# Performance work log

Hardware: AMD Instinct MI355X
Metric: run time of the kernel (lower is better)

Reference implementation:

```python
import jax, jax.numpy as jnp
import numpy as np
from functools import partial

N_NODES = 50000
N_EDGES = 800000
IN_F, HID_F, OUT_F = 128, 128, 64


def _linear_params(key, in_f, out_f):
    k1, k2 = jax.random.split(key)
    bound = 1.0 / np.sqrt(in_f)
    W = jax.random.uniform(k1, (out_f, in_f), jnp.float32, -bound, bound)
    b = jax.random.uniform(k2, (out_f,), jnp.float32, -bound, bound)
    return W, b


def setup_inputs() -> dict:
    key = jax.random.key(0)
    ks = jax.random.split(key, 10)
    features = jax.random.normal(ks[0], (N_NODES, IN_F), jnp.float32)
    src = jax.random.randint(ks[1], (N_EDGES,), 0, N_NODES, jnp.int32)
    dst = jax.random.randint(ks[2], (N_EDGES,), 0, N_NODES, jnp.int32)
    W1a, b1a = _linear_params(ks[3], IN_F, HID_F)
    W1b, b1b = _linear_params(ks[4], HID_F, HID_F)
    W2a, b2a = _linear_params(ks[5], HID_F, HID_F)
    W2b, b2b = _linear_params(ks[6], HID_F, HID_F)
    W3a, b3a = _linear_params(ks[7], HID_F, HID_F)
    W3b, b3b = _linear_params(ks[8], HID_F, OUT_F)
    return dict(features=features, src=src, dst=dst,
                W1a=W1a, b1a=b1a, W1b=W1b, b1b=b1b,
                W2a=W2a, b2a=b2a, W2b=W2b, b2b=b2b,
                W3a=W3a, b3a=b3a, W3b=W3b, b3b=b3b)


def _mean_agg(x, src, dst, n_nodes):
    # gather src features, segment-sum into dst, divide by in-degree (0-deg -> 0)
    summed = jax.ops.segment_sum(x[src], dst, num_segments=n_nodes)
    deg = jax.ops.segment_sum(jnp.ones((src.shape[0],), x.dtype), dst,
                              num_segments=n_nodes)
    return summed / jnp.maximum(deg, 1.0)[:, None]


def _gin_conv(x, src, dst, Wa, ba, Wb, bb):
    # DGL GINConv, aggregator 'mean', eps=0: h = MLP((1+eps)*x + mean_agg)
    h = x + _mean_agg(x, src, dst, x.shape[0])
    h = jax.nn.relu(h @ Wa.T + ba)
    return h @ Wb.T + bb


def reference(features, src, dst,
              W1a, b1a, W1b, b1b,
              W2a, b2a, W2b, b2b,
              W3a, b3a, W3b, b3b):
    x = jax.nn.relu(_gin_conv(features, src, dst, W1a, b1a, W1b, b1b))
    x = jax.nn.relu(_gin_conv(x, src, dst, W2a, b2a, W2b, b2b))
    x = jax.nn.relu(x @ W3a.T + b3a)
    return x @ W3b.T + b3b
```

## Files before the change

### kernel.cpp

```cpp
#include <hip/hip_runtime.h>
#include <hip/hip_fp16.h>

#define N_NODES 50000
#define N_EDGES 800000

typedef __attribute__((ext_vector_type(8))) short bf16x8;
typedef __attribute__((ext_vector_type(4))) float f32x4;

#define OFF_BUFA   0UL
#define OFF_T16    25600000UL
#define OFF_CNT    38400000UL
#define OFF_W      38600064UL
#define OFF_CSR    38960512UL

#define NB_EDGE 3125
#define NB_W    352
#define NB_FEAT 6250

__device__ __forceinline__ unsigned short bf16_rne(float f) {
  unsigned u = __float_as_uint(f);
  unsigned r = (u + 0x7FFFu + ((u >> 16) & 1u)) >> 16;
  return (unsigned short)r;
}

__device__ __forceinline__ int swz(int row, int b) {
  return (row * 256 + b) ^ ((row & 7) << 4);
}

__global__ __launch_bounds__(256)
void scatter16(const int* __restrict__ src, const int* __restrict__ dst,
               int* __restrict__ cnt, unsigned short* __restrict__ csr) {
  int i = blockIdx.x * 256 + threadIdx.x;
  int d = dst[i];
  int pos = atomicAdd(&cnt[d], 1);
  if (pos < 64) csr[(d << 6) + pos] = (unsigned short)src[i];
}

__global__ __launch_bounds__(256)
void conv_kernel(const float* __restrict__ W1a, const float* __restrict__ W1b,
                 const float* __restrict__ W2a, const float* __restrict__ W2b,
                 const float* __restrict__ W3a, const float* __restrict__ W3b,
                 unsigned short* __restrict__ pool,
                 const float* __restrict__ feat, __half* __restrict__ t16) {
  const int b = blockIdx.x;
  const int tid = threadIdx.x;
  if (b < NB_W) {
    int i = b * 256 + tid;
    const float* s;
    int base, local, msize;
    if (i < 16384)      { s = W1a; base = 0;      local = i;          msize = 16384; }
    else if (i < 32768) { s = W1b; base = 32768;  local = i - 16384;  msize = 16384; }
    else if (i < 49152) { s = W2a; base = 65536;  local = i - 32768;  msize = 16384; }
    else if (i < 65536) { s = W2b; base = 98304;  local = i - 49152;  msize = 16384; }
    else if (i < 81920) { s = W3a; base = 131072; local = i - 65536;  msize = 16384; }
    else                { s = W3b; base = 163840; local = i - 81920;  msize = 8192;  }
    float f = s[local];
    unsigned short hi = bf16_rne(f);
    float fh = __uint_as_float((unsigned)hi << 16);
    pool[base + local] = hi;
    pool[base + msize + local] = bf16_rne(f - fh);
  } else {
    int i = (b - NB_W) * 1024 + tid * 4;
    float4 v = *reinterpret_cast<const float4*>(feat + i);
    ushort4 h;
    h.x = __half_as_ushort(__float2half_rn(v.x));
    h.y = __half_as_ushort(__float2half_rn(v.y));
    h.z = __half_as_ushort(__float2half_rn(v.z));
    h.w = __half_as_ushort(__float2half_rn(v.w));
    *reinterpret_cast<ushort4*>((unsigned short*)t16 + i) = h;
  }
}

template <bool SELF32>
__global__ __launch_bounds__(256)
void agg_kernel(const __half* __restrict__ t16, const float* __restrict__ xself,
                const unsigned short* __restrict__ csr, const int* __restrict__ cnt,
                float* __restrict__ out) {
  int node = blockIdx.x * 4 + (threadIdx.x >> 6);
  if (node >= N_NODES) return;
  const int lane = threadIdx.x & 63;
  int deg = cnt[node];
  int dloop = min(deg, 64);
  int beg = node << 6;
  float inv = 1.0f / fmaxf((float)deg, 1.0f);

  float s0 = 0.f, s1 = 0.f, t0 = 0.f, t1 = 0.f;
  float u0 = 0.f, u1 = 0.f, v0 = 0.f, v1 = 0.f;
  int e = 0;
  for (; e + 3 < dloop; e += 4) {
    ushort4 q = *reinterpret_cast<const ushort4*>(csr + beg + e);
    float2 a = __half22float2(*reinterpret_cast<const __half2*>(t16 + (size_t)q.x * 128 + lane * 2));
    float2 b = __half22float2(*reinterpret_cast<const __half2*>(t16 + (size_t)q.y * 128 + lane * 2));
    float2 c = __half22float2(*reinterpret_cast<const __half2*>(t16 + (size_t)q.z * 128 + lane * 2));
    float2 d = __half22float2(*reinterpret_cast<const __half2*>(t16 + (size_t)q.w * 128 + lane * 2));
    s0 += a.x; s1 += a.y; t0 += b.x; t1 += b.y;
    u0 += c.x; u1 += c.y; v0 += d.x; v1 += d.y;
  }
  for (; e < dloop; ++e) {
    int i0 = csr[beg + e];
    float2 a = __half22float2(*reinterpret_cast<const __half2*>(t16 + (size_t)i0 * 128 + lane * 2));
    s0 += a.x; s1 += a.y;
  }
  float2 sm = make_float2(s0 + t0 + u0 + v0, s1 + t1 + u1 + v1);
  float2 xv;
  if (SELF32) {
    xv = *reinterpret_cast<const float2*>(xself + (size_t)node * 128 + lane * 2);
  } else {
    xv = __half22float2(*reinterpret_cast<const __half2*>(t16 + (size_t)node * 128 + lane * 2));
  }
  float2 o = make_float2(fmaf(sm.x, inv, xv.x), fmaf(sm.y, inv, xv.y));
  *reinterpret_cast<float2*>(out + (size_t)node * 128 + lane * 2) = o;
}

__device__ __forceinline__ void stage_x32(const float* __restrict__ X, int m0, int tid,
                                          char* ahi, char* alo, int M) {
  #pragma unroll
  for (int it = 0; it < 4; ++it) {
    int f = tid + it * 256;
    int row = f >> 5, c = f & 31;
    float4 v = make_float4(0.f, 0.f, 0.f, 0.f);
    if (m0 + row < M)
      v = *reinterpret_cast<const float4*>(X + (size_t)(m0 + row) * 128 + c * 4);
    ushort4 hi, lo;
    float fh;
    hi.x = bf16_rne(v.x); fh = __uint_as_float((unsigned)hi.x << 16); lo.x = bf16_rne(v.x - fh);
    hi.y = bf16_rne(v.y); fh = __uint_as_float((unsigned)hi.y << 16); lo.y = bf16_rne(v.y - fh);
    hi.z = bf16_rne(v.z); fh = __uint_as_float((unsigned)hi.z << 16); lo.z = bf16_rne(v.z - fh);
    hi.w = bf16_rne(v.w); fh = __uint_as_float((unsigned)hi.w << 16); lo.w = bf16_rne(v.w - fh);
    int bo = swz(row, c * 8);
    *reinterpret_cast<ushort4*>(ahi + bo) = hi;
    *reinterpret_cast<ushort4*>(alo + bo) = lo;
  }
}

template <int NB>
__device__ __forceinline__ void load_bfrag(const unsigned short* __restrict__ Wh,
                                           const unsigned short* __restrict__ Wl,
                                           int w, int lrow, int lg,
                                           bf16x8 (&bh)[NB][4], bf16x8 (&bl)[NB][4]) {
  #pragma unroll
  for (int nb = 0; nb < NB; ++nb) {
    int col = w * (16 * NB) + nb * 16 + lrow;
    #pragma unroll
    for (int kk = 0; kk < 4; ++kk) {
      int idx = col * 128 + kk * 32 + lg * 8;
      bh[nb][kk] = *reinterpret_cast<const bf16x8*>(Wh + idx);
      bl[nb][kk] = *reinterpret_cast<const bf16x8*>(Wl + idx);
    }
  }
}

template <int NB>
__device__ __forceinline__ void gemm_lds32(const char* ahi, const char* alo, int lrow, int lg,
                                           const bf16x8 (&bh)[NB][4], const bf16x8 (&bl)[NB][4],
                                           f32x4 (&acc)[2][NB]) {
  #pragma unroll
  for (int i = 0; i < 2; ++i)
    #pragma unroll
    for (int nb = 0; nb < NB; ++nb) acc[i][nb] = (f32x4){0.f, 0.f, 0.f, 0.f};
  #pragma unroll
  for (int i = 0; i < 2; ++i) {
    #pragma unroll
    for (int kk = 0; kk < 4; ++kk) {
      int bo = swz(i * 16 + lrow, kk * 64 + lg * 16);
      bf16x8 ah = *reinterpret_cast<const bf16x8*>(ahi + bo);
      bf16x8 al = *reinterpret_cast<const bf16x8*>(alo + bo);
      #pragma unroll
      for (int nb = 0; nb < NB; ++nb) {
        acc[i][nb] = __builtin_amdgcn_mfma_f32_16x16x32_bf16(ah, bh[nb][kk], acc[i][nb], 0, 0, 0);
        acc[i][nb] = __builtin_amdgcn_mfma_f32_16x16x32_bf16(al, bh[nb][kk], acc[i][nb], 0, 0, 0);
        acc[i][nb] = __builtin_amdgcn_mfma_f32_16x16x32_bf16(ah, bl[nb][kk], acc[i][nb], 0, 0, 0);
      }
    }
  }
}

__device__ __forceinline__ void store_h32(char* ahi, char* alo, const float* __restrict__ bias,
                                          int w, int lrow, int lg, f32x4 (&acc)[2][2]) {
  #pragma unroll
  for (int i = 0; i < 2; ++i) {
    #pragma unroll
    for (int nb = 0; nb < 2; ++nb) {
      int col = w * 32 + nb * 16 + lrow;
      float b = bias[col];
      #pragma unroll
      for (int r = 0; r < 4; ++r) {
        float v = fmaxf(acc[i][nb][r] + b, 0.f);
        int row = i * 16 + lg * 4 + r;
        unsigned short h = bf16_rne(v);
        float fh = __uint_as_float((unsigned)h << 16);
        unsigned short l2 = bf16_rne(v - fh);
        int bo = swz(row, col * 2);
        *reinterpret_cast<unsigned short*>(ahi + bo) = h;
        *reinterpret_cast<unsigned short*>(alo + bo) = l2;
      }
    }
  }
}

__global__ __launch_bounds__(256)
void mlp1_kernel(const float* __restrict__ X, const unsigned short* __restrict__ p,
                 const float* __restrict__ b1a, const float* __restrict__ b1b,
                 __half* __restrict__ Y, int M) {
  __shared__ unsigned short Ahi[32 * 128];
  __shared__ unsigned short Alo[32 * 128];
  char* ahi = (char*)Ahi;
  char* alo = (char*)Alo;
  const int tid = threadIdx.x;
  const int w = tid >> 6, l = tid & 63;
  const int lrow = l & 15, lg = l >> 4;
  const int m0 = blockIdx.x * 32;

  stage_x32(X, m0, tid, ahi, alo, M);
  __syncthreads();

  f32x4 acc[2][2];
  {
    bf16x8 bh[2][4], bl[2][4];
    load_bfrag<2>(p + 0, p + 16384, w, lrow, lg, bh, bl);
    gemm_lds32<2>(ahi, alo, lrow, lg, bh, bl, acc);
  }
  __syncthreads();
  {
    bf16x8 bh[2][4], bl[2][4];
    load_bfrag<2>(p + 32768, p + 49152, w, lrow, lg, bh, bl);
    store_h32(ahi, alo, b1a, w, lrow, lg, acc);
    __syncthreads();
    gemm_lds32<2>(ahi, alo, lrow, lg, bh, bl, acc);
  }
  #pragma unroll
  for (int i = 0; i < 2; ++i) {
    #pragma unroll
    for (int nb = 0; nb < 2; ++nb) {
      int col = w * 32 + nb * 16 + lrow;
      float b = b1b[col];
      #pragma unroll
      for (int r = 0; r < 4; ++r) {
        float v = fmaxf(acc[i][nb][r] + b, 0.f);
        int row = m0 + i * 16 + lg * 4 + r;
        if (row < M) Y[(size_t)row * 128 + col] = __float2half_rn(v);
      }
    }
  }
}

__global__ __launch_bounds__(256)
void mlp2head_kernel(const float* __restrict__ X, const unsigned short* __restrict__ p,
                     const float* __restrict__ b2a, const float* __restrict__ b2b,
                     const float* __restrict__ b3a, const float* __restrict__ b3b,
                     float* __restrict__ Y, int M) {
  __shared__ unsigned short Ahi[32 * 128];
  __shared__ unsigned short Alo[32 * 128];
  char* ahi = (char*)Ahi;
  char* alo = (char*)Alo;
  const int tid = threadIdx.x;
  const int w = tid >> 6, l = tid & 63;
  const int lrow = l & 15, lg = l >> 4;
  const int m0 = blockIdx.x * 32;

  stage_x32(X, m0, tid, ahi, alo, M);
  __syncthreads();

  f32x4 acc[2][2];
  {
    bf16x8 bh[2][4], bl[2][4];
    load_bfrag<2>(p + 65536, p + 81920, w, lrow, lg, bh, bl);
    gemm_lds32<2>(ahi, alo, lrow, lg, bh, bl, acc);
  }
  __syncthreads();
  {
    bf16x8 bh[2][4], bl[2][4];
    load_bfrag<2>(p + 98304, p + 114688, w, lrow, lg, bh, bl);
    store_h32(ahi, alo, b2a, w, lrow, lg, acc);
    __syncthreads();
    gemm_lds32<2>(ahi, alo, lrow, lg, bh, bl, acc);
  }
  __syncthreads();
  {
    bf16x8 bh[2][4], bl[2][4];
    load_bfrag<2>(p + 131072, p + 147456, w, lrow, lg, bh, bl);
    store_h32(ahi, alo, b2b, w, lrow, lg, acc);
    __syncthreads();
    gemm_lds32<2>(ahi, alo, lrow, lg, bh, bl, acc);
  }
  __syncthreads();
  f32x4 acc1[2][1];
  {
    bf16x8 bh[1][4], bl[1][4];
    load_bfrag<1>(p + 163840, p + 172032, w, lrow, lg, bh, bl);
    store_h32(ahi, alo, b3a, w, lrow, lg, acc);
    __syncthreads();
    gemm_lds32<1>(ahi, alo, lrow, lg, bh, bl, acc1);
  }
  #pragma unroll
  for (int i = 0; i < 2; ++i) {
    int col = w * 16 + lrow;
    float b = b3b[col];
    #pragma unroll
    for (int r = 0; r < 4; ++r) {
      float v = acc1[i][0][r] + b;
      int row = m0 + i * 16 + lg * 4 + r;
      if (row < M) Y[(size_t)row * 64 + col] = v;
    }
  }
}

extern "C" void kernel_launch(void* const* d_in, const int* in_sizes, int n_in,
                              void* d_out, int out_size, void* d_ws, size_t ws_size,
                              hipStream_t stream) {
  const float* feat = (const float*)d_in[0];
  const int*   esrc = (const int*)d_in[1];
  const int*   edst = (const int*)d_in[2];
  const float* W1a = (const float*)d_in[3];  const float* b1a = (const float*)d_in[4];
  const float* W1b = (const float*)d_in[5];  const float* b1b = (const float*)d_in[6];
  const float* W2a = (const float*)d_in[7];  const float* b2a = (const float*)d_in[8];
  const float* W2b = (const float*)d_in[9];  const float* b2b = (const float*)d_in[10];
  const float* W3a = (const float*)d_in[11]; const float* b3a = (const float*)d_in[12];
  const float* W3b = (const float*)d_in[13]; const float* b3b = (const float*)d_in[14];

  char* ws = (char*)d_ws;
  float*  bufA = (float*)(ws + OFF_BUFA);
  __half* t16  = (__half*)(ws + OFF_T16);
  int*    cnt  = (int*)(ws + OFF_CNT);
  unsigned short* p   = (unsigned short*)(ws + OFF_W);
  unsigned short* csr = (unsigned short*)(ws + OFF_CSR);

  hipMemsetAsync(cnt, 0, 200000, stream);

  scatter16<<<NB_EDGE, 256, 0, stream>>>(esrc, edst, cnt, csr);
  conv_kernel<<<NB_W + NB_FEAT, 256, 0, stream>>>(W1a, W1b, W2a, W2b, W3a, W3b, p, feat, t16);

  const int AB = (N_NODES + 3) / 4;
  const int GB = (N_NODES + 31) / 32;

  agg_kernel<true><<<AB, 256, 0, stream>>>(t16, feat, csr, cnt, bufA);
  mlp1_kernel<<<GB, 256, 0, stream>>>(bufA, p, b1a, b1b, t16, N_NODES);

  agg_kernel<false><<<AB, 256, 0, stream>>>(t16, feat, csr, cnt, bufA);
  mlp2head_kernel<<<GB, 256, 0, stream>>>(bufA, p, b2a, b2b, b3a, b3b,
                                          (float*)d_out, N_NODES);
}
```

Before: 224.3 us.

## Stage MLP weights into swizzled LDS via direct global-to-LDS loads

```diff
diff --git a/kernel.cpp b/kernel.cpp
--- a/kernel.cpp
+++ b/kernel.cpp
@@ -25,6 +25,12 @@
 
 __device__ __forceinline__ int swz(int row, int b) {
   return (row * 256 + b) ^ ((row & 7) << 4);
+}
+
+__device__ __forceinline__ void gload_lds16(const void* g, void* l) {
+  __builtin_amdgcn_global_load_lds(
+      (const __attribute__((address_space(1))) unsigned int*)g,
+      (__attribute__((address_space(3))) unsigned int*)l, 16, 0, 0);
 }
 
 __global__ __launch_bounds__(256)
@@ -133,43 +139,51 @@
   }
 }
 
+template <int NR>
+__device__ __forceinline__ void stage_w(const unsigned short* __restrict__ gh,
+                                        const unsigned short* __restrict__ gl,
+                                        char* WH, char* WL, int w, int lane) {
+  constexpr int CH = NR / 16;
+  #pragma unroll
+  for (int k = 0; k < CH; ++k) {
+    int base = w * (NR * 64) + k * 1024;
+    int ofs = base + lane * 16;
+    int row = ofs >> 8;
+    int g = ofs ^ ((row & 7) << 4);
+    gload_lds16((const char*)gh + g, WH + base);
+    gload_lds16((const char*)gl + g, WL + base);
+  }
+}
+
 template <int NB>
-__device__ __forceinline__ void load_bfrag(const unsigned short* __restrict__ Wh,
-                                           const unsigned short* __restrict__ Wl,
-                                           int w, int lrow, int lg,
-                                           bf16x8 (&bh)[NB][4], bf16x8 (&bl)[NB][4]) {
-  #pragma unroll
-  for (int nb = 0; nb < NB; ++nb) {
-    int col = w * (16 * NB) + nb * 16 + lrow;
-    #pragma unroll
-    for (int kk = 0; kk < 4; ++kk) {
-      int idx = col * 128 + kk * 32 + lg * 8;
-      bh[nb][kk] = *reinterpret_cast<const bf16x8*>(Wh + idx);
-      bl[nb][kk] = *reinterpret_cast<const bf16x8*>(Wl + idx);
-    }
-  }
-}
-
-template <int NB>
-__device__ __forceinline__ void gemm_lds32(const char* ahi, const char* alo, int lrow, int lg,
-                                           const bf16x8 (&bh)[NB][4], const bf16x8 (&bl)[NB][4],
-                                           f32x4 (&acc)[2][NB]) {
+__device__ __forceinline__ void gemm_ll(const char* ahi, const char* alo,
+                                        const char* wh, const char* wl,
+                                        int w, int lrow, int lg,
+                                        f32x4 (&acc)[2][NB]) {
   #pragma unroll
   for (int i = 0; i < 2; ++i)
     #pragma unroll
     for (int nb = 0; nb < NB; ++nb) acc[i][nb] = (f32x4){0.f, 0.f, 0.f, 0.f};
   #pragma unroll
-  for (int i = 0; i < 2; ++i) {
-    #pragma unroll
-    for (int kk = 0; kk < 4; ++kk) {
+  for (int kk = 0; kk < 4; ++kk) {
+    bf16x8 bh[NB], bl[NB];
+    #pragma unroll
+    for (int nb = 0; nb < NB; ++nb) {
+      int col = w * (16 * NB) + nb * 16 + lrow;
+      int wo = swz(col, kk * 64 + lg * 16);
+      bh[nb] = *reinterpret_cast<const bf16x8*>(wh + wo);
+      bl[nb] = *reinterpret_cast<const bf16x8*>(wl + wo);
+    }
+    #pragma unroll
+    for (int i = 0; i < 2; ++i) {
       int bo = swz(i * 16 + lrow, kk * 64 + lg * 16);
       bf16x8 ah = *reinterpret_cast<const bf16x8*>(ahi + bo);
       bf16x8 al = *reinterpret_cast<const bf16x8*>(alo + bo);
       #pragma unroll
       for (int nb = 0; nb < NB; ++nb) {
-        acc[i][nb] = __builtin_amdgcn_mfma_f32_16x16x32_bf16(ah, bh[nb][kk], acc[i][nb], 0, 0, 0);
-        acc[i][nb] = __builtin_amdgcn_mfma_f32_16x16x32_bf16(al, bh[nb][kk], acc[i][nb], 0, 0, 0);
-        acc[i][nb] = __builtin_amdgcn_mfma_f32_16x16x32_bf16(ah, bl[nb][kk], acc[i][nb], 0, 0, 0);
+        acc[i][nb] = __builtin_amdgcn_mfma_f32_16x16x32_bf16(ah, bh[nb], acc[i][nb], 0, 0, 0);
+        acc[i][nb] = __builtin_amdgcn_mfma_f32_16x16x32_bf16(al, bh[nb], acc[i][nb], 0, 0, 0);
+        acc[i][nb] = __builtin_amdgcn_mfma_f32_16x16x32_bf16(ah, bl[nb], acc[i][nb], 0, 0, 0);
       }
     }
   }
@@ -202,32 +216,33 @@
 void mlp1_kernel(const float* __restrict__ X, const unsigned short* __restrict__ p,
                  const float* __restrict__ b1a, const float* __restrict__ b1b,
                  __half* __restrict__ Y, int M) {
-  __shared__ unsigned short Ahi[32 * 128];
-  __shared__ unsigned short Alo[32 * 128];
+  __shared__ __align__(16) unsigned short Ahi[32 * 128];
+  __shared__ __align__(16) unsigned short Alo[32 * 128];
+  __shared__ __align__(16) unsigned short WHs[128 * 128];
+  __shared__ __align__(16) unsigned short WLs[128 * 128];
   char* ahi = (char*)Ahi;
   char* alo = (char*)Alo;
+  char* wh = (char*)WHs;
+  char* wl = (char*)WLs;
   const int tid = threadIdx.x;
   const int w = tid >> 6, l = tid & 63;
   const int lrow = l & 15, lg = l >> 4;
   const int m0 = blockIdx.x * 32;
 
+  stage_w<128>(p + 0, p + 16384, wh, wl, w, l);
   stage_x32(X, m0, tid, ahi, alo, M);
   __syncthreads();
 
   f32x4 acc[2][2];
-  {
-    bf16x8 bh[2][4], bl[2][4];
-    load_bfrag<2>(p + 0, p + 16384, w, lrow, lg, bh, bl);
-    gemm_lds32<2>(ahi, alo, lrow, lg, bh, bl, acc);
-  }
-  __syncthreads();
-  {
-    bf16x8 bh[2][4], bl[2][4];
-    load_bfrag<2>(p + 32768, p + 49152, w, lrow, lg, bh, bl);
-    store_h32(ahi, alo, b1a, w, lrow, lg, acc);
-    __syncthreads();
-    gemm_lds32<2>(ahi, alo, lrow, lg, bh, bl, acc);
-  }
+  gemm_ll<2>(ahi, alo, wh, wl, w, lrow, lg, acc);
+  __syncthreads();
+
+  stage_w<128>(p + 32768, p + 49152, wh, wl, w, l);
+  store_h32(ahi, alo, b1a, w, lrow, lg, acc);
+  __syncthreads();
+
+  gemm_ll<2>(ahi, alo, wh, wl, w, lrow, lg, acc);
+
   #pragma unroll
   for (int i = 0; i < 2; ++i) {
     #pragma unroll
@@ -249,49 +264,48 @@
                      const float* __restrict__ b2a, const float* __restrict__ b2b,
                      const float* __restrict__ b3a, const float* __restrict__ b3b,
                      float* __restrict__ Y, int M) {
-  __shared__ unsigned short Ahi[32 * 128];
-  __shared__ unsigned short Alo[32 * 128];
+  __shared__ __align__(16) unsigned short Ahi[32 * 128];
+  __shared__ __align__(16) unsigned short Alo[32 * 128];
+  __shared__ __align__(16) unsigned short WHs[128 * 128];
+  __shared__ __align__(16) unsigned short WLs[128 * 128];
   char* ahi = (char*)Ahi;
   char* alo = (char*)Alo;
+  char* wh = (char*)WHs;
+  char* wl = (char*)WLs;
   const int tid = threadIdx.x;
   const int w = tid >> 6, l = tid & 63;
   const int lrow = l & 15, lg = l >> 4;
   const int m0 = blockIdx.x * 32;
 
+  stage_w<128>(p + 65536, p + 81920, wh, wl, w, l);
   stage_x32(X, m0, tid, ahi, alo, M);
   __syncthreads();
 
   f32x4 acc[2][2];
-  {
-    bf16x8 bh[2][4], bl[2][4];
-    load_bfrag<2>(p + 65536, p + 81920, w, lrow, lg, bh, bl);
-    gemm_lds32<2>(ahi, alo, lrow, lg, bh, bl, acc);
-  }
-  __syncthreads();
-  {
-    bf16x8 bh[2][4], bl[2][4];
-    load_bfrag<2>(p + 98304, p + 114688, w, lrow, lg, bh, bl);
-    store_h32(ahi, alo, b2a, w, lrow, lg, acc);
-    __syncthreads();
-    gemm_lds32<2>(ahi, alo, lrow, lg, bh, bl, acc);
-  }
-  __syncthreads();
-  {
-    bf16x8 bh[2][4], bl[2][4];
-    load_bfrag<2>(p + 131072, p + 147456, w, lrow, lg, bh, bl);
-    store_h32(ahi, alo, b2b, w, lrow, lg, acc);
-    __syncthreads();
-    gemm_lds32<2>(ahi, alo, lrow, lg, bh, bl, acc);
-  }
-  __syncthreads();
+  gemm_ll<2>(ahi, alo, wh, wl, w, lrow, lg, acc);
+  __syncthreads();
+
+  stage_w<128>(p + 98304, p + 114688, wh, wl, w, l);
+  store_h32(ahi, alo, b2a, w, lrow, lg, acc);
+  __syncthreads();
+
+  gemm_ll<2>(ahi, alo, wh, wl, w, lrow, lg, acc);
+  __syncthreads();
+
+  stage_w<128>(p + 131072, p + 147456, wh, wl, w, l);
+  store_h32(ahi, alo, b2b, w, lrow, lg, acc);
+  __syncthreads();
+
+  gemm_ll<2>(ahi, alo, wh, wl, w, lrow, lg, acc);
+  __syncthreads();
+
+  stage_w<64>(p + 163840, p + 172032, wh, wl, w, l);
+  store_h32(ahi, alo, b3a, w, lrow, lg, acc);
+  __syncthreads();
+
   f32x4 acc1[2][1];
-  {
-    bf16x8 bh[1][4], bl[1][4];
-    load_bfrag<1>(p + 163840, p + 172032, w, lrow, lg, bh, bl);
-    store_h32(ahi, alo, b3a, w, lrow, lg, acc);
-    __syncthreads();
-    gemm_lds32<1>(ahi, alo, lrow, lg, bh, bl, acc1);
-  }
+  gemm_ll<1>(ahi, alo, wh, wl, w, lrow, lg, acc1);
+
   #pragma unroll
   for (int i = 0; i < 2; ++i) {
     int col = w * 16 + lrow;
```

Result: faster. 211.5 us (-5.7%).
